# Optimization experiments

Hardware: AMD Instinct MI355X
Metric: run time of the kernel (lower is better)

## Reference

```python
import jax, jax.numpy as jnp
import numpy as np

B = 524288   # batch rows
K = 8        # number of BooleanClassifiers
I = 64       # n_inputs
H = 32       # n_hidden
SCALE = 1.0  # LinearNetwork.scale (default [1.0])


def setup_inputs() -> dict:
    key = jax.random.key(0)
    k_x, k_w1, k_b1, k_w2, k_b2 = jax.random.split(key, 5)
    return {
        "x": jax.random.normal(k_x, (B, I), dtype=jnp.float32),
        "W1": jax.random.normal(k_w1, (K, H, I), dtype=jnp.float32) * 0.1,
        "b1": jax.random.normal(k_b1, (K, H), dtype=jnp.float32) * 0.1,
        "W2": jax.random.normal(k_w2, (K, H), dtype=jnp.float32) * 0.1,
        "b2": jax.random.normal(k_b2, (K,), dtype=jnp.float32) * 0.1,
        "bias": jnp.zeros((K,), dtype=jnp.float32),  # unused in training-mode forward
    }


def reference(x, W1, b1, W2, b2, bias):
    # Loop of K tiny Linear-Tanh-Linear-Tanh classifiers, fused as batched GEMMs.
    # h: [B, K, H]
    h = jnp.tanh(jnp.einsum("bi,khi->bkh", x, W1) + b1)
    # per-classifier scalar output, concatenated along dim=1 -> [B, K]
    out = jnp.tanh(jnp.einsum("bkh,kh->bk", h, W2) + b2)
    out = out * SCALE                   # LinearNetwork scale
    out = (out + 1.0) * 0.5 * SCALE     # LinearWithTanh training branch
    return out
```

## Files before the change

### kernel.cpp

```cpp
#include <hip/hip_runtime.h>

typedef __attribute__((ext_vector_type(8))) short short8;
typedef __attribute__((ext_vector_type(4))) float f32x4;

constexpr int GRID  = 8192;
constexpr float L2E2 = 2.8853900817779268f;

union V16 { uint4 u; short8 s; };

__device__ __forceinline__ unsigned pk(float lo, float hi) {
  const unsigned a = __float_as_uint(lo) + 0x8000u;
  const unsigned b = __float_as_uint(hi) + 0x8000u;
  return __builtin_amdgcn_perm(b, a, 0x07060302u);
}

__device__ __forceinline__ V16 pk8(f32x4 a, f32x4 b) {
  V16 v;
  v.u.x = pk(a[0], a[1]); v.u.y = pk(a[2], a[3]);
  v.u.z = pk(b[0], b[1]); v.u.w = pk(b[2], b[3]);
  return v;
}

__global__ __launch_bounds__(256, 4) void fused_mlp8(
    const float* __restrict__ x, const float* __restrict__ W1,
    const float* __restrict__ b1, const float* __restrict__ W2,
    const float* __restrict__ b2, float* __restrict__ out) {

  __shared__ V16 xb[512];

  const int tid  = threadIdx.x;
  const int wave = tid >> 6;
  const int lane = tid & 63;
  const int m16  = lane & 15;
  const int q    = lane >> 4;

  const int srow = tid >> 2;
  const int seg  = tid & 3;
  const int sw   = srow & 7;
  const float* gx = x + blockIdx.x * 4096 + srow * 64 + seg * 16;
  const f32x4 pf0 = *(const f32x4*)gx;
  const f32x4 pf1 = *(const f32x4*)(gx + 4);
  const f32x4 pf2 = *(const f32x4*)(gx + 8);
  const f32x4 pf3 = *(const f32x4*)(gx + 12);

  short8 w1f[4][2];
#pragma unroll
  for (int mt = 0; mt < 4; ++mt) {
    const int n = (wave * 4 + mt) * 16 + m16;
#pragma unroll
    for (int ks = 0; ks < 2; ++ks) {
      const float* p = W1 + n * 64 + ks * 32 + q * 8;
      const f32x4 u0 = *(const f32x4*)p, u1 = *(const f32x4*)(p + 4);
      f32x4 s0, s1;
#pragma unroll
      for (int r = 0; r < 4; ++r) { s0[r] = L2E2 * u0[r]; s1[r] = L2E2 * u1[r]; }
      w1f[mt][ks] = pk8(s0, s1).s;
    }
  }

  f32x4 kb1[4], w2q[4];
  float sw2[2] = {0.f, 0.f};
#pragma unroll
  for (int mt = 0; mt < 4; ++mt) {
    const int n0 = (wave * 4 + mt) * 16 + q * 4;
    const f32x4 b1x = *(const f32x4*)(b1 + n0);
    const f32x4 w2x = *(const f32x4*)(W2 + n0);
#pragma unroll
    for (int r = 0; r < 4; ++r) {
      kb1[mt][r] = L2E2 * b1x[r];
      w2q[mt][r] = (2.0f * L2E2) * w2x[r];
      sw2[mt >> 1] += w2x[r];
    }
  }
  float KSbn[2];
#pragma unroll
  for (int j = 0; j < 2; ++j) {
    float s = sw2[j];
    s += __shfl_xor(s, 16);
    s += __shfl_xor(s, 32);
    KSbn[j] = -0.25f * L2E2 * (s + b2[wave * 2 + j]);
  }

  xb[srow * 8 + ((seg * 2)     ^ sw)] = pk8(pf0, pf1);
  xb[srow * 8 + ((seg * 2 + 1) ^ sw)] = pk8(pf2, pf3);
  __syncthreads();

  const int obase = blockIdx.x * 512 + wave * 2;

#pragma unroll
  for (int tt = 0; tt < 4; ++tt) {
    const int r   = tt * 16 + m16;
    const int rsw = r & 7;
    const short8 xf0 = xb[r * 8 + (q       ^ rsw)].s;
    const short8 xf1 = xb[r * 8 + ((q + 4) ^ rsw)].s;

    f32x4 acc[4];
#pragma unroll
    for (int mt = 0; mt < 4; ++mt) {
      f32x4 z = kb1[mt];
      z = __builtin_amdgcn_mfma_f32_16x16x32_bf16(w1f[mt][0], xf0, z, 0, 0, 0);
      z = __builtin_amdgcn_mfma_f32_16x16x32_bf16(w1f[mt][1], xf1, z, 0, 0, 0);
      acc[mt] = z;
    }

    float o0 = 0.f, o1 = 0.f;
#pragma unroll
    for (int j = 0; j < 2; ++j) {
      float P = KSbn[j];
#pragma unroll
      for (int t = 0; t < 2; ++t) {
        const int mt = j * 2 + t;
        const float e0 = __builtin_amdgcn_exp2f(acc[mt][0]);
        const float e1 = __builtin_amdgcn_exp2f(acc[mt][1]);
        const float e2 = __builtin_amdgcn_exp2f(acc[mt][2]);
        const float e3 = __builtin_amdgcn_exp2f(acc[mt][3]);
        const float f0 = e0 + 1.0f, f1 = e1 + 1.0f;
        const float f2 = e2 + 1.0f, f3 = e3 + 1.0f;
        const float p01 = f0 * f1, p23 = f2 * f3;
        const float n01 = __builtin_fmaf(w2q[mt][0], f1, w2q[mt][1] * f0);
        const float n23 = __builtin_fmaf(w2q[mt][2], f3, w2q[mt][3] * f2);
        const float N   = __builtin_fmaf(n01, p23, n23 * p01);
        P = __builtin_fmaf(N, __builtin_amdgcn_rcpf(p01 * p23), P);
      }
      P += __shfl_xor(P, 16);
      P += __shfl_xor(P, 32);
      const float o = __builtin_amdgcn_rcpf(
          __builtin_amdgcn_exp2f(P) + 1.0f);
      if (j == 0) o0 = o; else o1 = o;
    }

    if (q == 0) {
      float2 st; st.x = o0; st.y = o1;
      *(float2*)(out + obase + r * 8) = st;
    }
  }
}

extern "C" void kernel_launch(void* const* d_in, const int* in_sizes, int n_in,
                              void* d_out, int out_size, void* d_ws, size_t ws_size,
                              hipStream_t stream) {
  const float* x  = (const float*)d_in[0];
  const float* W1 = (const float*)d_in[1];
  const float* b1 = (const float*)d_in[2];
  const float* W2 = (const float*)d_in[3];
  const float* b2 = (const float*)d_in[4];
  float* out = (float*)d_out;
  fused_mlp8<<<GRID, 256, 0, stream>>>(x, W1, b1, W2, b2, out);
}
```

Baseline: 237.3 us.

## Make blocks persistent with double-buffered x prefetch and one classifier per wave

```diff
diff --git a/kernel.cpp b/kernel.cpp
--- a/kernel.cpp
+++ b/kernel.cpp
@@ -3,8 +3,11 @@
 typedef __attribute__((ext_vector_type(8))) short short8;
 typedef __attribute__((ext_vector_type(4))) float f32x4;
 
-constexpr int GRID  = 8192;
-constexpr float L2E2 = 2.8853900817779268f;
+constexpr int B_ROWS   = 524288;
+constexpr int ROWTILES = B_ROWS / 64;
+constexpr int GRID     = 2048;
+constexpr int ITERS    = ROWTILES / GRID;
+constexpr float L2E2   = 2.8853900817779268f;
 
 union V16 { uint4 u; short8 s; };
 
@@ -21,12 +24,12 @@
   return v;
 }
 
-__global__ __launch_bounds__(256, 4) void fused_mlp8(
+__global__ __launch_bounds__(512, 4) void fused_mlp8(
     const float* __restrict__ x, const float* __restrict__ W1,
     const float* __restrict__ b1, const float* __restrict__ W2,
     const float* __restrict__ b2, float* __restrict__ out) {
 
-  __shared__ V16 xb[512];
+  __shared__ V16 xb[2][512];
 
   const int tid  = threadIdx.x;
   const int wave = tid >> 6;
@@ -34,19 +37,18 @@
   const int m16  = lane & 15;
   const int q    = lane >> 4;
 
-  const int srow = tid >> 2;
-  const int seg  = tid & 3;
+  const int srow = tid >> 3;
+  const int seg  = tid & 7;
   const int sw   = srow & 7;
-  const float* gx = x + blockIdx.x * 4096 + srow * 64 + seg * 16;
-  const f32x4 pf0 = *(const f32x4*)gx;
-  const f32x4 pf1 = *(const f32x4*)(gx + 4);
-  const f32x4 pf2 = *(const f32x4*)(gx + 8);
-  const f32x4 pf3 = *(const f32x4*)(gx + 12);
+  const float* gbase = x + (long)srow * 64 + seg * 8;
 
-  short8 w1f[4][2];
+  f32x4 pf0 = *(const f32x4*)(gbase + (long)blockIdx.x * 4096);
+  f32x4 pf1 = *(const f32x4*)(gbase + (long)blockIdx.x * 4096 + 4);
+
+  short8 w1f[2][2];
 #pragma unroll
-  for (int mt = 0; mt < 4; ++mt) {
-    const int n = (wave * 4 + mt) * 16 + m16;
+  for (int mt = 0; mt < 2; ++mt) {
+    const int n = wave * 32 + mt * 16 + m16;
 #pragma unroll
     for (int ks = 0; ks < 2; ++ks) {
       const float* p = W1 + n * 64 + ks * 32 + q * 8;
@@ -58,58 +60,54 @@
     }
   }
 
-  f32x4 kb1[4], w2q[4];
-  float sw2[2] = {0.f, 0.f};
+  f32x4 kb1[2], w2q[2];
+  float s = 0.f;
 #pragma unroll
-  for (int mt = 0; mt < 4; ++mt) {
-    const int n0 = (wave * 4 + mt) * 16 + q * 4;
+  for (int mt = 0; mt < 2; ++mt) {
+    const int n0 = wave * 32 + mt * 16 + q * 4;
     const f32x4 b1x = *(const f32x4*)(b1 + n0);
     const f32x4 w2x = *(const f32x4*)(W2 + n0);
 #pragma unroll
     for (int r = 0; r < 4; ++r) {
       kb1[mt][r] = L2E2 * b1x[r];
       w2q[mt][r] = (2.0f * L2E2) * w2x[r];
-      sw2[mt >> 1] += w2x[r];
+      s += w2x[r];
     }
   }
-  float KSbn[2];
-#pragma unroll
-  for (int j = 0; j < 2; ++j) {
-    float s = sw2[j];
-    s += __shfl_xor(s, 16);
-    s += __shfl_xor(s, 32);
-    KSbn[j] = -0.25f * L2E2 * (s + b2[wave * 2 + j]);
-  }
+  s += __shfl_xor(s, 16);
+  s += __shfl_xor(s, 32);
+  const float KSbn = -0.25f * L2E2 * (s + b2[wave]);
 
-  xb[srow * 8 + ((seg * 2)     ^ sw)] = pk8(pf0, pf1);
-  xb[srow * 8 + ((seg * 2 + 1) ^ sw)] = pk8(pf2, pf3);
+  xb[0][srow * 8 + (seg ^ sw)] = pk8(pf0, pf1);
+  pf0 = *(const f32x4*)(gbase + ((long)blockIdx.x + GRID) * 4096);
+  pf1 = *(const f32x4*)(gbase + ((long)blockIdx.x + GRID) * 4096 + 4);
   __syncthreads();
 
-  const int obase = blockIdx.x * 512 + wave * 2;
+#pragma unroll
+  for (int i = 0; i < ITERS; ++i) {
+    const int p = i & 1;
+    const long tile = (long)blockIdx.x + (long)i * GRID;
 
+    float osel = 0.f;
 #pragma unroll
-  for (int tt = 0; tt < 4; ++tt) {
-    const int r   = tt * 16 + m16;
-    const int rsw = r & 7;
-    const short8 xf0 = xb[r * 8 + (q       ^ rsw)].s;
-    const short8 xf1 = xb[r * 8 + ((q + 4) ^ rsw)].s;
+    for (int tt = 0; tt < 4; ++tt) {
+      const int r   = tt * 16 + m16;
+      const int rsw = r & 7;
+      const short8 xf0 = xb[p][r * 8 + (q       ^ rsw)].s;
+      const short8 xf1 = xb[p][r * 8 + ((q + 4) ^ rsw)].s;
 
-    f32x4 acc[4];
+      f32x4 acc[2];
 #pragma unroll
-    for (int mt = 0; mt < 4; ++mt) {
-      f32x4 z = kb1[mt];
-      z = __builtin_amdgcn_mfma_f32_16x16x32_bf16(w1f[mt][0], xf0, z, 0, 0, 0);
-      z = __builtin_amdgcn_mfma_f32_16x16x32_bf16(w1f[mt][1], xf1, z, 0, 0, 0);
-      acc[mt] = z;
-    }
+      for (int mt = 0; mt < 2; ++mt) {
+        f32x4 z = kb1[mt];
+        z = __builtin_amdgcn_mfma_f32_16x16x32_bf16(w1f[mt][0], xf0, z, 0, 0, 0);
+        z = __builtin_amdgcn_mfma_f32_16x16x32_bf16(w1f[mt][1], xf1, z, 0, 0, 0);
+        acc[mt] = z;
+      }
 
-    float o0 = 0.f, o1 = 0.f;
+      float P = KSbn;
 #pragma unroll
-    for (int j = 0; j < 2; ++j) {
-      float P = KSbn[j];
-#pragma unroll
-      for (int t = 0; t < 2; ++t) {
-        const int mt = j * 2 + t;
+      for (int mt = 0; mt < 2; ++mt) {
         const float e0 = __builtin_amdgcn_exp2f(acc[mt][0]);
         const float e1 = __builtin_amdgcn_exp2f(acc[mt][1]);
         const float e2 = __builtin_amdgcn_exp2f(acc[mt][2]);
@@ -124,14 +122,22 @@
       }
       P += __shfl_xor(P, 16);
       P += __shfl_xor(P, 32);
-      const float o = __builtin_amdgcn_rcpf(
-          __builtin_amdgcn_exp2f(P) + 1.0f);
-      if (j == 0) o0 = o; else o1 = o;
+      const float o = __builtin_amdgcn_rcpf(__builtin_amdgcn_exp2f(P) + 1.0f);
+      osel = (tt == q) ? o : osel;
     }
 
-    if (q == 0) {
-      float2 st; st.x = o0; st.y = o1;
-      *(float2*)(out + obase + r * 8) = st;
+    out[(tile * 64 + lane) * 8 + wave] = osel;
+
+    if (i + 1 < ITERS) {
+      xb[p ^ 1][srow * 8 + (seg ^ sw)] = pk8(pf0, pf1);
+    }
+
+    __syncthreads();
+
+    if (i + 2 < ITERS) {
+      const float* gp = gbase + (tile + 2 * GRID) * 4096;
+      pf0 = *(const f32x4*)gp;
+      pf1 = *(const f32x4*)(gp + 4);
     }
   }
 }
@@ -145,5 +151,5 @@
   const float* W2 = (const float*)d_in[3];
   const float* b2 = (const float*)d_in[4];
   float* out = (float*)d_out;
-  fused_mlp8<<<GRID, 256, 0, stream>>>(x, W1, b1, W2, b2, out);
+  fused_mlp8<<<GRID, 512, 0, stream>>>(x, W1, b1, W2, b2, out);
 }
```

After: 209.4 us. -11.8%, faster.
